# Kernel optimization log

Measured on AMD Instinct MI355X. Metric: run time of the kernel, lower is better.

## Reference

```python
import jax, jax.numpy as jnp
import numpy as np

TOP_K = 8
NEG_SLOPE = 0.2  # PyG GATConv default negative_slope


def setup_inputs() -> dict:
    key = jax.random.key(0)
    ks = jax.random.split(key, 8)
    B, C, T, D, H, KD = 16, 64, 128, 256, 8, 32
    s = 1.0 / np.sqrt(D)
    return {
        "x": jax.random.normal(ks[0], (B, C, T, D), jnp.float32),
        "static_adj": jax.random.normal(ks[1], (C, C), jnp.float32),
        "w_q": jax.random.normal(ks[2], (KD, D), jnp.float32) * s,
        "w_k": jax.random.normal(ks[3], (KD, D), jnp.float32) * s,
        "gat_lin": jax.random.normal(ks[4], (H * D, D), jnp.float32) * s,  # shared lin_src/lin_dst
        "att_src": jax.random.normal(ks[5], (H, D), jnp.float32) * s,
        "att_dst": jax.random.normal(ks[6], (H, D), jnp.float32) * s,
        "gat_bias": jnp.zeros((D,), jnp.float32),
    }


def reference(x, static_adj, w_q, w_k, gat_lin, att_src, att_dst, gat_bias):
    B, C, T, D = x.shape
    H = att_src.shape[0]
    kd = w_q.shape[0]

    # ---- dynamic adjacency ----
    h = x.mean(axis=2)                                   # [B,C,D] temporal summary
    q = h @ w_q.T                                        # [B,C,KD]
    k = h @ w_k.T                                        # [B,C,KD]
    sim = jnp.einsum('bik,bjk->bij', q, k) / np.float32(np.sqrt(kd))
    delta_a = jnp.tanh(sim)                              # [B,C,C]
    adaptive = static_adj[None] + delta_a                # [B,C,C]

    # top-k per row -> sparse mask (edge: row i = source, col j = target, per dense_to_sparse)
    _, idx = jax.lax.top_k(jnp.abs(adaptive), TOP_K)     # [B,C,K]
    mask = jnp.any(jax.nn.one_hot(idx, C, dtype=bool), axis=-2)  # [B,C,C]
    mask = mask | jnp.eye(C, dtype=bool)                 # GATConv add_self_loops=True

    # ---- GAT message passing (dense masked attention, graph shared across T) ----
    xt = jnp.swapaxes(x, 1, 2)                           # [B,T,C,D]
    wx = (xt @ gat_lin.T).reshape(B, T, C, H, D)         # [B,T,C,H,F]
    a_s = jnp.einsum('btchf,hf->btch', wx, att_src)      # source term
    a_d = jnp.einsum('btchf,hf->btch', wx, att_dst)      # target term
    # e[b,t,i,j,h]: edge source i -> target j
    e = a_s[:, :, :, None, :] + a_d[:, :, None, :, :]
    e = jax.nn.leaky_relu(e, NEG_SLOPE)
    e = jnp.where(mask[:, None, :, :, None], e, -jnp.inf)
    alpha = jax.nn.softmax(e, axis=2)                    # softmax over incoming sources i per target j
    out = jnp.einsum('btijh,btihf->btjhf', alpha, wx)    # aggregate messages
    out = out.mean(axis=3) + gat_bias                    # concat=False -> mean heads, add bias
    x_updated = jnp.swapaxes(out, 1, 2)                  # [B,C,T,D]
    return x_updated, delta_a
```

## Files before the change

### kernel.cpp

```cpp
#include <hip/hip_runtime.h>

typedef _Float16 h2_t __attribute__((ext_vector_type(2)));
typedef _Float16 h4_t __attribute__((ext_vector_type(4)));
typedef _Float16 h8_t __attribute__((ext_vector_type(8)));
typedef __fp16 fp16x2 __attribute__((ext_vector_type(2)));
typedef float f32x16 __attribute__((ext_vector_type(16)));


__device__ __forceinline__ h2_t pkrtz(float a, float b) {
  union { fp16x2 f; h2_t h; } u;
  u.f = __builtin_amdgcn_cvt_pkrtz(a, b);
  return u.h;
}

__device__ __forceinline__ unsigned pk_u(float a, float b) {
  union { fp16x2 f; unsigned u; } z;
  z.f = __builtin_amdgcn_cvt_pkrtz(a, b);
  return z.u;
}

__device__ __forceinline__ h8_t mk8(unsigned w0, unsigned w1, unsigned w2, unsigned w3) {
  union { unsigned u[4]; h8_t h; } z;
  z.u[0] = w0; z.u[1] = w1; z.u[2] = w2; z.u[3] = w3;
  return z.h;
}

__device__ __forceinline__ float fdot2_(h2_t a, h2_t b, float c) {
#if __has_builtin(__builtin_amdgcn_fdot2)
  return __builtin_amdgcn_fdot2(a, b, c, false);
#else
  return fmaf((float)a[0], (float)b[0], fmaf((float)a[1], (float)b[1], c));
#endif
}

__device__ __forceinline__ h2_t u2h(unsigned u) {
  union { unsigned u; h2_t h; } x; x.u = u; return x.h;
}

__global__ void k_hmean(const float* __restrict__ x, float* __restrict__ h) {
  __shared__ float4 red[256];
  int bc = blockIdx.x;
  int d4 = threadIdx.x & 63;
  int tq = threadIdx.x >> 6;
  const float4* xp = (const float4*)(x + (size_t)bc * 32768) + d4;
  float4 s = {0.f, 0.f, 0.f, 0.f};
  #pragma unroll 8
  for (int t = 0; t < 32; ++t) {
    float4 v = xp[(size_t)(tq * 32 + t) * 64];
    s.x += v.x; s.y += v.y; s.z += v.z; s.w += v.w;
  }
  red[threadIdx.x] = s;
  __syncthreads();
  if (tq == 0) {
    float4 a = red[d4], b = red[64 + d4], c = red[128 + d4], d = red[192 + d4];
    float4 o;
    o.x = (a.x + b.x + c.x + d.x) * (1.f / 128.f);
    o.y = (a.y + b.y + c.y + d.y) * (1.f / 128.f);
    o.z = (a.z + b.z + c.z + d.z) * (1.f / 128.f);
    o.w = (a.w + b.w + c.w + d.w) * (1.f / 128.f);
    ((float4*)(h + bc * 256))[d4] = o;
  }
}

__global__ void k_qk(const float* __restrict__ h, const float* __restrict__ wq,
                     const float* __restrict__ wk, float* __restrict__ q,
                     float* __restrict__ k) {
  int gid = blockIdx.x * 256 + threadIdx.x;
  int isK = gid >> 15;
  int e = gid & 32767;
  int kk = e & 31;
  int bi = e >> 5;
  const float4* h4 = (const float4*)(h + bi * 256);
  const float4* w4 = (const float4*)((isK ? wk : wq) + kk * 256);
  float s = 0.f;
  #pragma unroll 4
  for (int d = 0; d < 64; ++d) {
    float4 a = h4[d], bv = w4[d];
    s = fmaf(a.x, bv.x, s); s = fmaf(a.y, bv.y, s);
    s = fmaf(a.z, bv.z, s); s = fmaf(a.w, bv.w, s);
  }
  (isK ? k : q)[e] = s;
}

__global__ void k_adj(const float* __restrict__ q, const float* __restrict__ k,
                      const float* __restrict__ sadj, float* __restrict__ dout,
                      unsigned long long* __restrict__ cmask) {
  __shared__ float qs[64][33], ks[64][33];
  __shared__ float ad[64][65];
  __shared__ unsigned long long rowm[64];
  int b = blockIdx.x, tid = threadIdx.x;
  for (int r = 0; r < 8; ++r) {
    int idx = r * 256 + tid;
    qs[idx >> 5][idx & 31] = q[b * 2048 + idx];
    ks[idx >> 5][idx & 31] = k[b * 2048 + idx];
  }
  __syncthreads();
  const float rs = 0.17677669529663687f;
  for (int r = 0; r < 16; ++r) {
    int idx = r * 256 + tid;
    int i = idx >> 6, j = idx & 63;
    float s = 0.f;
    #pragma unroll 8
    for (int kk = 0; kk < 32; ++kk) s = fmaf(qs[i][kk], ks[j][kk], s);
    float dv = tanhf(s * rs);
    dout[b * 4096 + idx] = dv;
    ad[i][j] = sadj[idx] + dv;
  }
  __syncthreads();
  if (tid < 64) {
    unsigned long long sel = 0ull;
    for (int p = 0; p < 8; ++p) {
      float best = -1.f; int bj = 0;
      for (int j = 0; j < 64; ++j) {
        if ((sel >> j) & 1ull) continue;
        float v = fabsf(ad[tid][j]);
        if (v > best) { best = v; bj = j; }
      }
      sel |= 1ull << bj;
    }
    rowm[tid] = sel;
  }
  __syncthreads();
  if (tid < 64) {
    unsigned long long cmv = 1ull << tid;
    for (int i = 0; i < 64; ++i) cmv |= ((rowm[i] >> tid) & 1ull) << i;
    cmask[b * 64 + tid] = cmv;
  }
}

__global__ void k_vsd(const float* __restrict__ glin, const float* __restrict__ asrc,
                      const float* __restrict__ adst, _Float16* __restrict__ vsd16) {
  int hh = blockIdx.x, d = threadIdx.x;
  const float* gb = glin + (size_t)hh * 65536;
  float s = 0.f, t = 0.f;
  for (int f = 0; f < 256; ++f) {
    float g = gb[f * 256 + d];
    s = fmaf(asrc[hh * 256 + f], g, s);
    t = fmaf(adst[hh * 256 + f], g, t);
  }
  vsd16[hh * 256 + d] = (_Float16)s;
  vsd16[(8 + hh) * 256 + d] = (_Float16)t;
}

__global__ void k_grearr(const float* __restrict__ g, _Float16* __restrict__ o) {
  int gid = blockIdx.x * 256 + threadIdx.x;
  int lane = gid & 63;
  int fg = (gid >> 6) & 3;
  int FID = gid >> 8;
  int ft = FID & 1, kk = (FID >> 1) & 3, s = FID >> 3;
  int h = s >> 2, dc = s & 3;
  int l5 = lane & 31, hi = lane >> 5;
  int f = fg * 64 + ft * 32 + l5;
  int d0 = dc * 64 + kk * 16 + hi * 8;
  const float* src = g + ((size_t)(h * 256 + f) << 8) + d0;
  float4 a = *(const float4*)src;
  float4 bq = *(const float4*)(src + 4);
  h8_t v;
  v[0] = (_Float16)a.x;  v[1] = (_Float16)a.y;  v[2] = (_Float16)a.z;  v[3] = (_Float16)a.w;
  v[4] = (_Float16)bq.x; v[5] = (_Float16)bq.y; v[6] = (_Float16)bq.z; v[7] = (_Float16)bq.w;
  *(h8_t*)(o + (size_t)gid * 8) = v;
}

__global__ __launch_bounds__(512) void k_main(
    const float* __restrict__ x, const _Float16* __restrict__ vsd16,
    const unsigned long long* __restrict__ cmask,
    const _Float16* __restrict__ g16r, const float* __restrict__ bias,
    float* __restrict__ out)
{
  __shared__ __align__(16) char LDS[69632];
  char* XR  = LDS;
  char* PT  = LDS;
  char* RED = LDS;
  float* ASp = (float*)(LDS + 65536);
  float* ADp = (float*)(LDS + 67584);

  const int tid = threadIdx.x;
  const int lane = tid & 63;
  const int w = __builtin_amdgcn_readfirstlane(tid >> 6);
  const int hi = lane >> 5;
  const int l5 = lane & 31;
  const int l7 = lane & 7;
  const int mg = w & 1;
  const int fg = w >> 1;
  const int bt = blockIdx.x;
  const int b = bt >> 7, t = bt & 127;

  const char* gb0 = (const char*)g16r + fg * 1024 + lane * 16;

  h8_t GA[8], GB[8];
  #pragma unroll
  for (int q = 0; q < 8; ++q) GA[q] = *(const h8_t*)(gb0 + q * 4096);

  #pragma unroll
  for (int r = 0; r < 8; ++r) {
    int i = w * 8 + r;
    const float4 v = *(const float4*)(x + (((size_t)(b * 64 + i) * 128 + t) << 8) + lane * 4);
    h2_t p0 = pkrtz(v.x, v.y);
    h2_t p1 = pkrtz(v.z, v.w);
    h4_t hv; hv[0] = p0[0]; hv[1] = p0[1]; hv[2] = p1[0]; hv[3] = p1[1];
    int db = lane >> 1;
    int off = i * 512 + (((db & 24) | ((db ^ (i & 7)) & 7)) << 4) + ((lane & 1) << 3);
    *(h4_t*)(XR + off) = hv;
  }
  __syncthreads();

  h8_t Af[16];
  {
    int i = mg * 32 + l5;
    #pragma unroll
    for (int k = 0; k < 16; ++k) {
      int db = k * 2 + hi;
      Af[k] = *(const h8_t*)(XR + i * 512 + (((db & 24) | ((db ^ l7) & 7)) << 4));
    }
  }

  {
    float a_s = 0.f, a_d = 0.f;
    const unsigned* vsp = (const unsigned*)vsd16 + w * 128;
    const unsigned* vdp = (const unsigned*)vsd16 + (8 + w) * 128;
    #pragma unroll 4
    for (int db = 0; db < 32; ++db) {
      h8_t xv = *(const h8_t*)(XR + lane * 512 + (((db & 24) | ((db ^ l7) & 7)) << 4));
      #pragma unroll
      for (int c = 0; c < 4; ++c) {
        h2_t x2; x2[0] = xv[c * 2]; x2[1] = xv[c * 2 + 1];
        a_s = fdot2_(x2, u2h(vsp[db * 4 + c]), a_s);
        a_d = fdot2_(x2, u2h(vdp[db * 4 + c]), a_d);
      }
    }
    ASp[w * 64 + lane] = a_s;
    ADp[w * 64 + lane] = a_d;
  }
  __syncthreads();

  {
    const unsigned long long cmj = cmask[b * 64 + lane];
    const float adj = ADp[w * 64 + lane];
    const float* asr = ASp + w * 64;
    float ssum = 0.f;
    #pragma unroll 8
    for (int i = 0; i < 64; ++i) {
      float e = asr[i] + adj;
      e = fmaxf(e, 0.f) + 0.2f * fminf(e, 0.f);
      e = ((cmj >> i) & 1ull) ? e : -1e30f;
      ssum += exp2f(e * 1.44269504f);
    }
    const float rinv = 1.f / ssum;
    #pragma unroll
    for (int c = 0; c < 8; ++c) {
      float vv[8];
      #pragma unroll
      for (int e8 = 0; e8 < 8; ++e8) {
        int i = c * 8 + e8;
        float e = asr[i] + adj;
        e = fmaxf(e, 0.f) + 0.2f * fminf(e, 0.f);
        e = ((cmj >> i) & 1ull) ? e : -1e30f;
        vv[e8] = exp2f(e * 1.44269504f) * rinv;
      }
      *(h8_t*)(PT + w * 8192 + lane * 128 + ((c ^ l7) << 4)) =
          mk8(pk_u(vv[0], vv[1]), pk_u(vv[2], vv[3]),
              pk_u(vv[4], vv[5]), pk_u(vv[6], vv[7]));
    }
  }
  __syncthreads();

  f32x16 acc00 = {}, acc01 = {}, acc10 = {}, acc11 = {};

  #pragma unroll 1
  for (int h = 0; h < 8; ++h) {
    f32x16 d0 = {}, d1 = {};

    #pragma unroll
    for (int dc = 0; dc < 4; ++dc) {
      const int s = h * 4 + dc;
      const int sp = (s < 31) ? s + 1 : 31;
      const char* gpp = gb0 + (size_t)sp * 32768;
      if ((dc & 1) == 0) {
        #pragma unroll
        for (int q = 0; q < 8; ++q) GB[q] = *(const h8_t*)(gpp + q * 4096);
        __builtin_amdgcn_s_setprio(1);
        #pragma unroll
        for (int kk = 0; kk < 4; ++kk) {
          d0 = __builtin_amdgcn_mfma_f32_32x32x16_f16(Af[dc * 4 + kk], GA[kk * 2 + 0], d0, 0, 0, 0);
          d1 = __builtin_amdgcn_mfma_f32_32x32x16_f16(Af[dc * 4 + kk], GA[kk * 2 + 1], d1, 0, 0, 0);
        }
        __builtin_amdgcn_s_setprio(0);
      } else {
        #pragma unroll
        for (int q = 0; q < 8; ++q) GA[q] = *(const h8_t*)(gpp + q * 4096);
        __builtin_amdgcn_s_setprio(1);
        #pragma unroll
        for (int kk = 0; kk < 4; ++kk) {
          d0 = __builtin_amdgcn_mfma_f32_32x32x16_f16(Af[dc * 4 + kk], GB[kk * 2 + 0], d0, 0, 0, 0);
          d1 = __builtin_amdgcn_mfma_f32_32x32x16_f16(Af[dc * 4 + kk], GB[kk * 2 + 1], d1, 0, 0, 0);
        }
        __builtin_amdgcn_s_setprio(0);
      }
    }

    h8_t B2[2][2];
    {
      const bool H = (hi != 0);
      #pragma unroll
      for (int ft = 0; ft < 2; ++ft) {
        const f32x16& dd = ft ? d1 : d0;
        unsigned P0 = pk_u(dd[0], dd[1]),  P1 = pk_u(dd[2], dd[3]);
        unsigned P2 = pk_u(dd[4], dd[5]),  P3 = pk_u(dd[6], dd[7]);
        unsigned P4 = pk_u(dd[8], dd[9]),  P5 = pk_u(dd[10], dd[11]);
        unsigned P6 = pk_u(dd[12], dd[13]), P7 = pk_u(dd[14], dd[15]);
        {
          unsigned Pa = H ? P2 : P0, Pb = H ? P3 : P1;
          unsigned Qa = H ? P0 : P2, Qb = H ? P1 : P3;
          unsigned S0 = (unsigned)__shfl_xor((int)Qa, 32);
          unsigned S1 = (unsigned)__shfl_xor((int)Qb, 32);
          B2[0][ft] = mk8(H ? S0 : Pa, H ? S1 : Pb, H ? Pa : S0, H ? Pb : S1);
        }
        {
          unsigned Pa = H ? P6 : P4, Pb = H ? P7 : P5;
          unsigned Qa = H ? P4 : P6, Qb = H ? P5 : P7;
          unsigned S0 = (unsigned)__shfl_xor((int)Qa, 32);
          unsigned S1 = (unsigned)__shfl_xor((int)Qb, 32);
          B2[1][ft] = mk8(H ? S0 : Pa, H ? S1 : Pb, H ? Pa : S0, H ? Pb : S1);
        }
      }
    }

    h8_t A2[2][2];
    #pragma unroll
    for (int jt = 0; jt < 2; ++jt)
      #pragma unroll
      for (int kbl = 0; kbl < 2; ++kbl) {
        int c = mg * 4 + kbl * 2 + hi;
        A2[jt][kbl] = *(const h8_t*)(PT + h * 8192 + (jt * 32 + l5) * 128 + ((c ^ (l5 & 7)) << 4));
      }

    __builtin_amdgcn_s_setprio(1);
    acc00 = __builtin_amdgcn_mfma_f32_32x32x16_f16(A2[0][0], B2[0][0], acc00, 0, 0, 0);
    acc00 = __builtin_amdgcn_mfma_f32_32x32x16_f16(A2[0][1], B2[1][0], acc00, 0, 0, 0);
    acc01 = __builtin_amdgcn_mfma_f32_32x32x16_f16(A2[0][0], B2[0][1], acc01, 0, 0, 0);
    acc01 = __builtin_amdgcn_mfma_f32_32x32x16_f16(A2[0][1], B2[1][1], acc01, 0, 0, 0);
    acc10 = __builtin_amdgcn_mfma_f32_32x32x16_f16(A2[1][0], B2[0][0], acc10, 0, 0, 0);
    acc10 = __builtin_amdgcn_mfma_f32_32x32x16_f16(A2[1][1], B2[1][0], acc10, 0, 0, 0);
    acc11 = __builtin_amdgcn_mfma_f32_32x32x16_f16(A2[1][0], B2[0][1], acc11, 0, 0, 0);
    acc11 = __builtin_amdgcn_mfma_f32_32x32x16_f16(A2[1][1], B2[1][1], acc11, 0, 0, 0);
    __builtin_amdgcn_s_setprio(0);
  }

  __syncthreads();
  if (mg == 1) {
    #pragma unroll
    for (int jt = 0; jt < 2; ++jt)
      #pragma unroll
      for (int ft = 0; ft < 2; ++ft) {
        const f32x16& a = jt ? (ft ? acc11 : acc10) : (ft ? acc01 : acc00);
        #pragma unroll
        for (int rq = 0; rq < 4; ++rq) {
          float4 v; v.x = a[rq*4+0]; v.y = a[rq*4+1]; v.z = a[rq*4+2]; v.w = a[rq*4+3];
          *(float4*)(RED + (((((fg*2+jt)*2+ft)*4 + rq)*64 + lane) << 4)) = v;
        }
      }
  }
  __syncthreads();
  if (mg == 0) {
    const float bi0 = bias[fg * 64 + l5];
    const float bi1 = bias[fg * 64 + 32 + l5];
    float* ob = out + ((size_t)(b * 64) * 128 + t) * 256;
    #pragma unroll
    for (int jt = 0; jt < 2; ++jt)
      #pragma unroll
      for (int ft = 0; ft < 2; ++ft) {
        const f32x16& a = jt ? (ft ? acc11 : acc10) : (ft ? acc01 : acc00);
        const float bv = ft ? bi1 : bi0;
        const int fcol = fg * 64 + ft * 32 + l5;
        #pragma unroll
        for (int rq = 0; rq < 4; ++rq) {
          float4 p = *(const float4*)(RED + (((((fg*2+jt)*2+ft)*4 + rq)*64 + lane) << 4));
          #pragma unroll
          for (int rr = 0; rr < 4; ++rr) {
            int j = jt * 32 + rr + 8 * rq + 4 * hi;
            float sum = a[rq*4+rr] + ((const float*)&p)[rr];
            ob[(size_t)j * 32768 + fcol] = sum * 0.125f + bv;
          }
        }
      }
  }
}

extern "C" void kernel_launch(void* const* d_in, const int* in_sizes, int n_in,
                              void* d_out, int out_size, void* d_ws, size_t ws_size,
                              hipStream_t stream) {
  const float* x    = (const float*)d_in[0];
  const float* sadj = (const float*)d_in[1];
  const float* wq   = (const float*)d_in[2];
  const float* wk   = (const float*)d_in[3];
  const float* glin = (const float*)d_in[4];
  const float* asrc = (const float*)d_in[5];
  const float* adst = (const float*)d_in[6];
  const float* bias = (const float*)d_in[7];

  float* out = (float*)d_out;
  float* delta_out = out + (size_t)16 * 64 * 128 * 256;

  char* ws = (char*)d_ws;
  float* h   = (float*)(ws + 0);
  float* q   = (float*)(ws + 1048576);
  float* k   = (float*)(ws + 1179648);
  unsigned long long* cm = (unsigned long long*)(ws + 1310720);
  _Float16* vsd16 = (_Float16*)(ws + 1318912);
  _Float16* g16r  = (_Float16*)(ws + 1327104);

  hipLaunchKernelGGL(k_hmean,  dim3(1024), dim3(256), 0, stream, x, h);
  hipLaunchKernelGGL(k_qk,     dim3(256),  dim3(256), 0, stream, h, wq, wk, q, k);
  hipLaunchKernelGGL(k_adj,    dim3(16),   dim3(256), 0, stream, q, k, sadj, delta_out, cm);
  hipLaunchKernelGGL(k_vsd,    dim3(8),    dim3(256), 0, stream, glin, asrc, adst, vsd16);
  hipLaunchKernelGGL(k_grearr, dim3(256),  dim3(256), 0, stream, glin, g16r);
  hipLaunchKernelGGL(k_main,   dim3(2048), dim3(512), 0, stream, x, vsd16, cm, g16r, bias, out);
}
```

Measured before the change: 374.6 us.

## Split work by feature tile per wave to cut registers and drop LDS reduction

Each wave now owns one 32-wide feature tile across all 64 nodes, instead of splitting nodes into two groups that are later summed through LDS. X fragments are read from LDS on demand rather than held in 16 registers, and the double-buffered G prefetch is removed. The softmax tables are built in two rounds of four heads into a separate LDS region, and launch bounds now request 4 waves per SIMD for higher occupancy. The cost is more LDS reads, extra barriers between rounds, and global G loads that are no longer prefetched ahead of the MFMAs.

```diff
diff --git a/kernel.cpp b/kernel.cpp
--- a/kernel.cpp
+++ b/kernel.cpp
@@ -161,7 +161,7 @@
   *(h8_t*)(o + (size_t)gid * 8) = v;
 }
 
-__global__ __launch_bounds__(512) void k_main(
+__global__ __launch_bounds__(512, 4) void k_main(
     const float* __restrict__ x, const _Float16* __restrict__ vsd16,
     const unsigned long long* __restrict__ cmask,
     const _Float16* __restrict__ g16r, const float* __restrict__ bias,
@@ -169,8 +169,7 @@
 {
   __shared__ __align__(16) char LDS[69632];
   char* XR  = LDS;
-  char* PT  = LDS;
-  char* RED = LDS;
+  char* PT  = LDS + 32768;
   float* ASp = (float*)(LDS + 65536);
   float* ADp = (float*)(LDS + 67584);
 
@@ -180,16 +179,14 @@
   const int hi = lane >> 5;
   const int l5 = lane & 31;
   const int l7 = lane & 7;
-  const int mg = w & 1;
   const int fg = w >> 1;
+  const int ft = w & 1;
   const int bt = blockIdx.x;
   const int b = bt >> 7, t = bt & 127;
 
-  const char* gb0 = (const char*)g16r + fg * 1024 + lane * 16;
-
-  h8_t GA[8], GB[8];
-  #pragma unroll
-  for (int q = 0; q < 8; ++q) GA[q] = *(const h8_t*)(gb0 + q * 4096);
+  const char* gb0 = (const char*)g16r + fg * 1024 + ft * 4096 + lane * 16;
+
+  const unsigned long long cmj = cmask[b * 64 + lane];
 
   #pragma unroll
   for (int r = 0; r < 8; ++r) {
@@ -203,16 +200,6 @@
     *(h4_t*)(XR + off) = hv;
   }
   __syncthreads();
-
-  h8_t Af[16];
-  {
-    int i = mg * 32 + l5;
-    #pragma unroll
-    for (int k = 0; k < 16; ++k) {
-      int db = k * 2 + hi;
-      Af[k] = *(const h8_t*)(XR + i * 512 + (((db & 24) | ((db ^ l7) & 7)) << 4));
-    }
-  }
 
   {
     float a_s = 0.f, a_d = 0.f;
@@ -233,155 +220,161 @@
   }
   __syncthreads();
 
-  {
-    const unsigned long long cmj = cmask[b * 64 + lane];
-    const float adj = ADp[w * 64 + lane];
-    const float* asr = ASp + w * 64;
-    float ssum = 0.f;
-    #pragma unroll 8
-    for (int i = 0; i < 64; ++i) {
-      float e = asr[i] + adj;
-      e = fmaxf(e, 0.f) + 0.2f * fminf(e, 0.f);
-      e = ((cmj >> i) & 1ull) ? e : -1e30f;
-      ssum += exp2f(e * 1.44269504f);
-    }
-    const float rinv = 1.f / ssum;
-    #pragma unroll
-    for (int c = 0; c < 8; ++c) {
-      float vv[8];
-      #pragma unroll
-      for (int e8 = 0; e8 < 8; ++e8) {
-        int i = c * 8 + e8;
+  f32x16 acc0 = {}, acc1 = {};
+
+  #pragma unroll 1
+  for (int rnd = 0; rnd < 2; ++rnd) {
+    if (w < 4) {
+      const int h = rnd * 4 + w;
+      const float adj = ADp[h * 64 + lane];
+      const float* asr = ASp + h * 64;
+      float ssum = 0.f;
+      #pragma unroll 8
+      for (int i = 0; i < 64; ++i) {
         float e = asr[i] + adj;
         e = fmaxf(e, 0.f) + 0.2f * fminf(e, 0.f);
         e = ((cmj >> i) & 1ull) ? e : -1e30f;
-        vv[e8] = exp2f(e * 1.44269504f) * rinv;
-      }
-      *(h8_t*)(PT + w * 8192 + lane * 128 + ((c ^ l7) << 4)) =
-          mk8(pk_u(vv[0], vv[1]), pk_u(vv[2], vv[3]),
-              pk_u(vv[4], vv[5]), pk_u(vv[6], vv[7]));
+        ssum += exp2f(e * 1.44269504f);
+      }
+      const float rinv = 1.f / ssum;
+      char* pslot = PT + w * 8192;
+      #pragma unroll
+      for (int c = 0; c < 8; ++c) {
+        float vv[8];
+        #pragma unroll
+        for (int e8 = 0; e8 < 8; ++e8) {
+          int i = c * 8 + e8;
+          float e = asr[i] + adj;
+          e = fmaxf(e, 0.f) + 0.2f * fminf(e, 0.f);
+          e = ((cmj >> i) & 1ull) ? e : -1e30f;
+          vv[e8] = exp2f(e * 1.44269504f) * rinv;
+        }
+        *(h8_t*)(pslot + lane * 128 + ((c ^ l7) << 4)) =
+            mk8(pk_u(vv[0], vv[1]), pk_u(vv[2], vv[3]),
+                pk_u(vv[4], vv[5]), pk_u(vv[6], vv[7]));
+      }
     }
-  }
-  __syncthreads();
-
-  f32x16 acc00 = {}, acc01 = {}, acc10 = {}, acc11 = {};
-
-  #pragma unroll 1
-  for (int h = 0; h < 8; ++h) {
-    f32x16 d0 = {}, d1 = {};
-
-    #pragma unroll
-    for (int dc = 0; dc < 4; ++dc) {
-      const int s = h * 4 + dc;
-      const int sp = (s < 31) ? s + 1 : 31;
-      const char* gpp = gb0 + (size_t)sp * 32768;
-      if ((dc & 1) == 0) {
-        #pragma unroll
-        for (int q = 0; q < 8; ++q) GB[q] = *(const h8_t*)(gpp + q * 4096);
-        __builtin_amdgcn_s_setprio(1);
-        #pragma unroll
-        for (int kk = 0; kk < 4; ++kk) {
-          d0 = __builtin_amdgcn_mfma_f32_32x32x16_f16(Af[dc * 4 + kk], GA[kk * 2 + 0], d0, 0, 0, 0);
-          d1 = __builtin_amdgcn_mfma_f32_32x32x16_f16(Af[dc * 4 + kk], GA[kk * 2 + 1], d1, 0, 0, 0);
-        }
-        __builtin_amdgcn_s_setprio(0);
-      } else {
-        #pragma unroll
-        for (int q = 0; q < 8; ++q) GA[q] = *(const h8_t*)(gpp + q * 4096);
-        __builtin_amdgcn_s_setprio(1);
-        #pragma unroll
-        for (int kk = 0; kk < 4; ++kk) {
-          d0 = __builtin_amdgcn_mfma_f32_32x32x16_f16(Af[dc * 4 + kk], GB[kk * 2 + 0], d0, 0, 0, 0);
-          d1 = __builtin_amdgcn_mfma_f32_32x32x16_f16(Af[dc * 4 + kk], GB[kk * 2 + 1], d1, 0, 0, 0);
-        }
-        __builtin_amdgcn_s_setprio(0);
-      }
-    }
-
-    h8_t B2[2][2];
-    {
-      const bool H = (hi != 0);
+    __syncthreads();
+
+    #pragma unroll 1
+    for (int hh = 0; hh < 4; ++hh) {
+      const int h = rnd * 4 + hh;
+      f32x16 d0 = {}, d1 = {};
+
       #pragma unroll
-      for (int ft = 0; ft < 2; ++ft) {
-        const f32x16& dd = ft ? d1 : d0;
-        unsigned P0 = pk_u(dd[0], dd[1]),  P1 = pk_u(dd[2], dd[3]);
-        unsigned P2 = pk_u(dd[4], dd[5]),  P3 = pk_u(dd[6], dd[7]);
-        unsigned P4 = pk_u(dd[8], dd[9]),  P5 = pk_u(dd[10], dd[11]);
-        unsigned P6 = pk_u(dd[12], dd[13]), P7 = pk_u(dd[14], dd[15]);
+      for (int dc = 0; dc < 4; ++dc) {
+        const int s = h * 4 + dc;
+        const char* gpp = gb0 + (size_t)s * 32768;
+        h8_t G0 = *(const h8_t*)(gpp);
+        h8_t G1 = *(const h8_t*)(gpp + 8192);
+        h8_t G2 = *(const h8_t*)(gpp + 16384);
+        h8_t G3 = *(const h8_t*)(gpp + 24576);
         {
-          unsigned Pa = H ? P2 : P0, Pb = H ? P3 : P1;
-          unsigned Qa = H ? P0 : P2, Qb = H ? P1 : P3;
-          unsigned S0 = (unsigned)__shfl_xor((int)Qa, 32);
-          unsigned S1 = (unsigned)__shfl_xor((int)Qb, 32);
-          B2[0][ft] = mk8(H ? S0 : Pa, H ? S1 : Pb, H ? Pa : S0, H ? Pb : S1);
+          h8_t a0, a1, a2, a3;
+          {
+            int db = dc * 8 + 0 * 2 + hi;
+            a0 = *(const h8_t*)(XR + l5 * 512 + (((db & 24) | ((db ^ l7) & 7)) << 4));
+            db = dc * 8 + 1 * 2 + hi;
+            a1 = *(const h8_t*)(XR + l5 * 512 + (((db & 24) | ((db ^ l7) & 7)) << 4));
+            db = dc * 8 + 2 * 2 + hi;
+            a2 = *(const h8_t*)(XR + l5 * 512 + (((db & 24) | ((db ^ l7) & 7)) << 4));
+            db = dc * 8 + 3 * 2 + hi;
+            a3 = *(const h8_t*)(XR + l5 * 512 + (((db & 24) | ((db ^ l7) & 7)) << 4));
+          }
+          d0 = __builtin_amdgcn_mfma_f32_32x32x16_f16(a0, G0, d0, 0, 0, 0);
+          d0 = __builtin_amdgcn_mfma_f32_32x32x16_f16(a1, G1, d0, 0, 0, 0);
+          d0 = __builtin_amdgcn_mfma_f32_32x32x16_f16(a2, G2, d0, 0, 0, 0);
+          d0 = __builtin_amdgcn_mfma_f32_32x32x16_f16(a3, G3, d0, 0, 0, 0);
         }
         {
-          unsigned Pa = H ? P6 : P4, Pb = H ? P7 : P5;
-          unsigned Qa = H ? P4 : P6, Qb = H ? P5 : P7;
-          unsigned S0 = (unsigned)__shfl_xor((int)Qa, 32);
-          unsigned S1 = (unsigned)__shfl_xor((int)Qb, 32);
-          B2[1][ft] = mk8(H ? S0 : Pa, H ? S1 : Pb, H ? Pa : S0, H ? Pb : S1);
+          h8_t a0, a1, a2, a3;
+          {
+            int db = dc * 8 + 0 * 2 + hi;
+            a0 = *(const h8_t*)(XR + (32 + l5) * 512 + (((db & 24) | ((db ^ l7) & 7)) << 4));
+            db = dc * 8 + 1 * 2 + hi;
+            a1 = *(const h8_t*)(XR + (32 + l5) * 512 + (((db & 24) | ((db ^ l7) & 7)) << 4));
+            db = dc * 8 + 2 * 2 + hi;
+            a2 = *(const h8_t*)(XR + (32 + l5) * 512 + (((db & 24) | ((db ^ l7) & 7)) << 4));
+            db = dc * 8 + 3 * 2 + hi;
+            a3 = *(const h8_t*)(XR + (32 + l5) * 512 + (((db & 24) | ((db ^ l7) & 7)) << 4));
+          }
+          d1 = __builtin_amdgcn_mfma_f32_32x32x16_f16(a0, G0, d1, 0, 0, 0);
+          d1 = __builtin_amdgcn_mfma_f32_32x32x16_f16(a1, G1, d1, 0, 0, 0);
+          d1 = __builtin_amdgcn_mfma_f32_32x32x16_f16(a2, G2, d1, 0, 0, 0);
+          d1 = __builtin_amdgcn_mfma_f32_32x32x16_f16(a3, G3, d1, 0, 0, 0);
         }
       }
+
+      h8_t B20, B21, B22, B23;
+      {
+        const bool H = (hi != 0);
+        {
+          unsigned P0 = pk_u(d0[0], d0[1]),  P1 = pk_u(d0[2], d0[3]);
+          unsigned P2 = pk_u(d0[4], d0[5]),  P3 = pk_u(d0[6], d0[7]);
+          unsigned P4 = pk_u(d0[8], d0[9]),  P5 = pk_u(d0[10], d0[11]);
+          unsigned P6 = pk_u(d0[12], d0[13]), P7 = pk_u(d0[14], d0[15]);
+          {
+            unsigned Pa = H ? P2 : P0, Pb = H ? P3 : P1;
+            unsigned Qa = H ? P0 : P2, Qb = H ? P1 : P3;
+            unsigned S0 = (unsigned)__shfl_xor((int)Qa, 32);
+            unsigned S1 = (unsigned)__shfl_xor((int)Qb, 32);
+            B20 = mk8(H ? S0 : Pa, H ? S1 : Pb, H ? Pa : S0, H ? Pb : S1);
+          }
+          {
+            unsigned Pa = H ? P6 : P4, Pb = H ? P7 : P5;
+            unsigned Qa = H ? P4 : P6, Qb = H ? P5 : P7;
+            unsigned S0 = (unsigned)__shfl_xor((int)Qa, 32);
+            unsigned S1 = (unsigned)__shfl_xor((int)Qb, 32);
+            B21 = mk8(H ? S0 : Pa, H ? S1 : Pb, H ? Pa : S0, H ? Pb : S1);
+          }
+        }
+        {
+          unsigned P0 = pk_u(d1[0], d1[1]),  P1 = pk_u(d1[2], d1[3]);
+          unsigned P2 = pk_u(d1[4], d1[5]),  P3 = pk_u(d1[6], d1[7]);
+          unsigned P4 = pk_u(d1[8], d1[9]),  P5 = pk_u(d1[10], d1[11]);
+          unsigned P6 = pk_u(d1[12], d1[13]), P7 = pk_u(d1[14], d1[15]);
+          {
+            unsigned Pa = H ? P2 : P0, Pb = H ? P3 : P1;
+            unsigned Qa = H ? P0 : P2, Qb = H ? P1 : P3;
+            unsigned S0 = (unsigned)__shfl_xor((int)Qa, 32);
+            unsigned S1 = (unsigned)__shfl_xor((int)Qb, 32);
+            B22 = mk8(H ? S0 : Pa, H ? S1 : Pb, H ? Pa : S0, H ? Pb : S1);
+          }
+          {
+            unsigned Pa = H ? P6 : P4, Pb = H ? P7 : P5;
+            unsigned Qa = H ? P4 : P6, Qb = H ? P5 : P7;
+            unsigned S0 = (unsigned)__shfl_xor((int)Qa, 32);
+            unsigned S1 = (unsigned)__shfl_xor((int)Qb, 32);
+            B23 = mk8(H ? S0 : Pa, H ? S1 : Pb, H ? Pa : S0, H ? Pb : S1);
+          }
+        }
+      }
+
+      const char* pslot = PT + hh * 8192;
+      #pragma unroll
+      for (int kbl = 0; kbl < 4; ++kbl) {
+        const int c = kbl * 2 + hi;
+        h8_t a20 = *(const h8_t*)(pslot + l5 * 128 + ((c ^ (l5 & 7)) << 4));
+        h8_t a21 = *(const h8_t*)(pslot + (32 + l5) * 128 + ((c ^ (l5 & 7)) << 4));
+        const h8_t bb = (kbl == 0) ? B20 : (kbl == 1) ? B21 : (kbl == 2) ? B22 : B23;
+        acc0 = __builtin_amdgcn_mfma_f32_32x32x16_f16(a20, bb, acc0, 0, 0, 0);
+        acc1 = __builtin_amdgcn_mfma_f32_32x32x16_f16(a21, bb, acc1, 0, 0, 0);
+      }
     }
-
-    h8_t A2[2][2];
-    #pragma unroll
-    for (int jt = 0; jt < 2; ++jt)
-      #pragma unroll
-      for (int kbl = 0; kbl < 2; ++kbl) {
-        int c = mg * 4 + kbl * 2 + hi;
-        A2[jt][kbl] = *(const h8_t*)(PT + h * 8192 + (jt * 32 + l5) * 128 + ((c ^ (l5 & 7)) << 4));
-      }
-
-    __builtin_amdgcn_s_setprio(1);
-    acc00 = __builtin_amdgcn_mfma_f32_32x32x16_f16(A2[0][0], B2[0][0], acc00, 0, 0, 0);
-    acc00 = __builtin_amdgcn_mfma_f32_32x32x16_f16(A2[0][1], B2[1][0], acc00, 0, 0, 0);
-    acc01 = __builtin_amdgcn_mfma_f32_32x32x16_f16(A2[0][0], B2[0][1], acc01, 0, 0, 0);
-    acc01 = __builtin_amdgcn_mfma_f32_32x32x16_f16(A2[0][1], B2[1][1], acc01, 0, 0, 0);
-    acc10 = __builtin_amdgcn_mfma_f32_32x32x16_f16(A2[1][0], B2[0][0], acc10, 0, 0, 0);
-    acc10 = __builtin_amdgcn_mfma_f32_32x32x16_f16(A2[1][1], B2[1][0], acc10, 0, 0, 0);
-    acc11 = __builtin_amdgcn_mfma_f32_32x32x16_f16(A2[1][0], B2[0][1], acc11, 0, 0, 0);
-    acc11 = __builtin_amdgcn_mfma_f32_32x32x16_f16(A2[1][1], B2[1][1], acc11, 0, 0, 0);
-    __builtin_amdgcn_s_setprio(0);
-  }
-
-  __syncthreads();
-  if (mg == 1) {
-    #pragma unroll
-    for (int jt = 0; jt < 2; ++jt)
-      #pragma unroll
-      for (int ft = 0; ft < 2; ++ft) {
-        const f32x16& a = jt ? (ft ? acc11 : acc10) : (ft ? acc01 : acc00);
-        #pragma unroll
-        for (int rq = 0; rq < 4; ++rq) {
-          float4 v; v.x = a[rq*4+0]; v.y = a[rq*4+1]; v.z = a[rq*4+2]; v.w = a[rq*4+3];
-          *(float4*)(RED + (((((fg*2+jt)*2+ft)*4 + rq)*64 + lane) << 4)) = v;
-        }
-      }
-  }
-  __syncthreads();
-  if (mg == 0) {
-    const float bi0 = bias[fg * 64 + l5];
-    const float bi1 = bias[fg * 64 + 32 + l5];
+    __syncthreads();
+  }
+
+  {
+    const int fcol = w * 32 + l5;
+    const float bv = bias[fcol];
     float* ob = out + ((size_t)(b * 64) * 128 + t) * 256;
     #pragma unroll
-    for (int jt = 0; jt < 2; ++jt)
+    for (int rq = 0; rq < 4; ++rq)
       #pragma unroll
-      for (int ft = 0; ft < 2; ++ft) {
-        const f32x16& a = jt ? (ft ? acc11 : acc10) : (ft ? acc01 : acc00);
-        const float bv = ft ? bi1 : bi0;
-        const int fcol = fg * 64 + ft * 32 + l5;
-        #pragma unroll
-        for (int rq = 0; rq < 4; ++rq) {
-          float4 p = *(const float4*)(RED + (((((fg*2+jt)*2+ft)*4 + rq)*64 + lane) << 4));
-          #pragma unroll
-          for (int rr = 0; rr < 4; ++rr) {
-            int j = jt * 32 + rr + 8 * rq + 4 * hi;
-            float sum = a[rq*4+rr] + ((const float*)&p)[rr];
-            ob[(size_t)j * 32768 + fcol] = sum * 0.125f + bv;
-          }
-        }
+      for (int rr = 0; rr < 4; ++rr) {
+        int j0 = rq * 8 + hi * 4 + rr;
+        ob[(size_t)j0 * 32768 + fcol]        = acc0[rq * 4 + rr] * 0.125f + bv;
+        ob[(size_t)(32 + j0) * 32768 + fcol] = acc1[rq * 4 + rr] * 0.125f + bv;
       }
   }
 }
```

Result: slower. 737.9 us (+97.0%).

## Fuse q/k projection into adjacency kernel, merge weight prep kernels, drop setprio

Applied to the files above, without the earlier changes.

Folds the q/k projection into the adjacency/top-k kernel, so each of 16 blocks loads its h rows into LDS and computes q and k there instead of in a separate launch. Also merges the weight rearrangement and attention-vector kernels into one launch, and removes the s_setprio hints around the MFMA sequences in the main kernel. The aim is to cut launch overhead and intermediate global traffic. The cost is that the q/k work now runs on only 16 blocks with a large LDS footprint, which can serialize it, and losing the priority hints may change how MFMA work interleaves across waves.

```diff
diff --git a/kernel.cpp b/kernel.cpp
--- a/kernel.cpp
+++ b/kernel.cpp
@@ -62,39 +62,44 @@
   }
 }
 
-__global__ void k_qk(const float* __restrict__ h, const float* __restrict__ wq,
-                     const float* __restrict__ wk, float* __restrict__ q,
-                     float* __restrict__ k) {
-  int gid = blockIdx.x * 256 + threadIdx.x;
-  int isK = gid >> 15;
-  int e = gid & 32767;
-  int kk = e & 31;
-  int bi = e >> 5;
-  const float4* h4 = (const float4*)(h + bi * 256);
-  const float4* w4 = (const float4*)((isK ? wk : wq) + kk * 256);
-  float s = 0.f;
-  #pragma unroll 4
-  for (int d = 0; d < 64; ++d) {
-    float4 a = h4[d], bv = w4[d];
-    s = fmaf(a.x, bv.x, s); s = fmaf(a.y, bv.y, s);
-    s = fmaf(a.z, bv.z, s); s = fmaf(a.w, bv.w, s);
-  }
-  (isK ? k : q)[e] = s;
-}
-
-__global__ void k_adj(const float* __restrict__ q, const float* __restrict__ k,
-                      const float* __restrict__ sadj, float* __restrict__ dout,
-                      unsigned long long* __restrict__ cmask) {
+__global__ void k_adjq(const float* __restrict__ h, const float* __restrict__ wq,
+                       const float* __restrict__ wk, const float* __restrict__ sadj,
+                       float* __restrict__ dout, unsigned long long* __restrict__ cmask) {
+  __shared__ float hs[64][256];
   __shared__ float qs[64][33], ks[64][33];
   __shared__ float ad[64][65];
   __shared__ unsigned long long rowm[64];
   int b = blockIdx.x, tid = threadIdx.x;
-  for (int r = 0; r < 8; ++r) {
-    int idx = r * 256 + tid;
-    qs[idx >> 5][idx & 31] = q[b * 2048 + idx];
-    ks[idx >> 5][idx & 31] = k[b * 2048 + idx];
-  }
-  __syncthreads();
+
+  {
+    const float4* hp = (const float4*)(h + (size_t)b * 16384);
+    #pragma unroll
+    for (int r = 0; r < 16; ++r) {
+      int idx = r * 256 + tid;
+      ((float4*)&hs[idx >> 6][0])[idx & 63] = hp[idx];
+    }
+  }
+  __syncthreads();
+
+  #pragma unroll
+  for (int r = 0; r < 16; ++r) {
+    int e = r * 256 + tid;
+    int isK = e >> 11;
+    int rest = e & 2047;
+    int i = rest >> 5, kk = rest & 31;
+    const float4* hv = (const float4*)&hs[i][0];
+    const float4* wv = (const float4*)((isK ? wk : wq) + kk * 256);
+    float s = 0.f;
+    #pragma unroll 4
+    for (int d = 0; d < 64; ++d) {
+      float4 a = hv[d], bv = wv[d];
+      s = fmaf(a.x, bv.x, s); s = fmaf(a.y, bv.y, s);
+      s = fmaf(a.z, bv.z, s); s = fmaf(a.w, bv.w, s);
+    }
+    (isK ? ks : qs)[i][kk] = s;
+  }
+  __syncthreads();
+
   const float rs = 0.17677669529663687f;
   for (int r = 0; r < 16; ++r) {
     int idx = r * 256 + tid;
@@ -128,37 +133,38 @@
   }
 }
 
-__global__ void k_vsd(const float* __restrict__ glin, const float* __restrict__ asrc,
-                      const float* __restrict__ adst, _Float16* __restrict__ vsd16) {
-  int hh = blockIdx.x, d = threadIdx.x;
-  const float* gb = glin + (size_t)hh * 65536;
-  float s = 0.f, t = 0.f;
-  for (int f = 0; f < 256; ++f) {
-    float g = gb[f * 256 + d];
-    s = fmaf(asrc[hh * 256 + f], g, s);
-    t = fmaf(adst[hh * 256 + f], g, t);
-  }
-  vsd16[hh * 256 + d] = (_Float16)s;
-  vsd16[(8 + hh) * 256 + d] = (_Float16)t;
-}
-
-__global__ void k_grearr(const float* __restrict__ g, _Float16* __restrict__ o) {
-  int gid = blockIdx.x * 256 + threadIdx.x;
-  int lane = gid & 63;
-  int fg = (gid >> 6) & 3;
-  int FID = gid >> 8;
-  int ft = FID & 1, kk = (FID >> 1) & 3, s = FID >> 3;
-  int h = s >> 2, dc = s & 3;
-  int l5 = lane & 31, hi = lane >> 5;
-  int f = fg * 64 + ft * 32 + l5;
-  int d0 = dc * 64 + kk * 16 + hi * 8;
-  const float* src = g + ((size_t)(h * 256 + f) << 8) + d0;
-  float4 a = *(const float4*)src;
-  float4 bq = *(const float4*)(src + 4);
-  h8_t v;
-  v[0] = (_Float16)a.x;  v[1] = (_Float16)a.y;  v[2] = (_Float16)a.z;  v[3] = (_Float16)a.w;
-  v[4] = (_Float16)bq.x; v[5] = (_Float16)bq.y; v[6] = (_Float16)bq.z; v[7] = (_Float16)bq.w;
-  *(h8_t*)(o + (size_t)gid * 8) = v;
+__global__ void k_prep(const float* __restrict__ g, const float* __restrict__ asrc,
+                       const float* __restrict__ adst, _Float16* __restrict__ o,
+                       _Float16* __restrict__ vsd16) {
+  if (blockIdx.x < 256) {
+    int gid = blockIdx.x * 256 + threadIdx.x;
+    int lane = gid & 63;
+    int fg = (gid >> 6) & 3;
+    int FID = gid >> 8;
+    int ft = FID & 1, kk = (FID >> 1) & 3, s = FID >> 3;
+    int h = s >> 2, dc = s & 3;
+    int l5 = lane & 31, hi = lane >> 5;
+    int f = fg * 64 + ft * 32 + l5;
+    int d0 = dc * 64 + kk * 16 + hi * 8;
+    const float* src = g + ((size_t)(h * 256 + f) << 8) + d0;
+    float4 a = *(const float4*)src;
+    float4 bq = *(const float4*)(src + 4);
+    h8_t v;
+    v[0] = (_Float16)a.x;  v[1] = (_Float16)a.y;  v[2] = (_Float16)a.z;  v[3] = (_Float16)a.w;
+    v[4] = (_Float16)bq.x; v[5] = (_Float16)bq.y; v[6] = (_Float16)bq.z; v[7] = (_Float16)bq.w;
+    *(h8_t*)(o + (size_t)gid * 8) = v;
+  } else {
+    int hh = blockIdx.x - 256, d = threadIdx.x;
+    const float* gb = g + (size_t)hh * 65536;
+    float s = 0.f, t = 0.f;
+    for (int f = 0; f < 256; ++f) {
+      float gv = gb[f * 256 + d];
+      s = fmaf(asrc[hh * 256 + f], gv, s);
+      t = fmaf(adst[hh * 256 + f], gv, t);
+    }
+    vsd16[hh * 256 + d] = (_Float16)s;
+    vsd16[(8 + hh) * 256 + d] = (_Float16)t;
+  }
 }
 
 __global__ __launch_bounds__(512) void k_main(
@@ -278,23 +284,19 @@
       if ((dc & 1) == 0) {
         #pragma unroll
         for (int q = 0; q < 8; ++q) GB[q] = *(const h8_t*)(gpp + q * 4096);
-        __builtin_amdgcn_s_setprio(1);
         #pragma unroll
         for (int kk = 0; kk < 4; ++kk) {
           d0 = __builtin_amdgcn_mfma_f32_32x32x16_f16(Af[dc * 4 + kk], GA[kk * 2 + 0], d0, 0, 0, 0);
           d1 = __builtin_amdgcn_mfma_f32_32x32x16_f16(Af[dc * 4 + kk], GA[kk * 2 + 1], d1, 0, 0, 0);
         }
-        __builtin_amdgcn_s_setprio(0);
       } else {
         #pragma unroll
         for (int q = 0; q < 8; ++q) GA[q] = *(const h8_t*)(gpp + q * 4096);
-        __builtin_amdgcn_s_setprio(1);
         #pragma unroll
         for (int kk = 0; kk < 4; ++kk) {
           d0 = __builtin_amdgcn_mfma_f32_32x32x16_f16(Af[dc * 4 + kk], GB[kk * 2 + 0], d0, 0, 0, 0);
           d1 = __builtin_amdgcn_mfma_f32_32x32x16_f16(Af[dc * 4 + kk], GB[kk * 2 + 1], d1, 0, 0, 0);
         }
-        __builtin_amdgcn_s_setprio(0);
       }
     }
 
@@ -334,7 +336,6 @@
         A2[jt][kbl] = *(const h8_t*)(PT + h * 8192 + (jt * 32 + l5) * 128 + ((c ^ (l5 & 7)) << 4));
       }
 
-    __builtin_amdgcn_s_setprio(1);
     acc00 = __builtin_amdgcn_mfma_f32_32x32x16_f16(A2[0][0], B2[0][0], acc00, 0, 0, 0);
     acc00 = __builtin_amdgcn_mfma_f32_32x32x16_f16(A2[0][1], B2[1][0], acc00, 0, 0, 0);
     acc01 = __builtin_amdgcn_mfma_f32_32x32x16_f16(A2[0][0], B2[0][1], acc01, 0, 0, 0);
@@ -343,7 +344,6 @@
     acc10 = __builtin_amdgcn_mfma_f32_32x32x16_f16(A2[1][1], B2[1][0], acc10, 0, 0, 0);
     acc11 = __builtin_amdgcn_mfma_f32_32x32x16_f16(A2[1][0], B2[0][1], acc11, 0, 0, 0);
     acc11 = __builtin_amdgcn_mfma_f32_32x32x16_f16(A2[1][1], B2[1][1], acc11, 0, 0, 0);
-    __builtin_amdgcn_s_setprio(0);
   }
 
   __syncthreads();
@@ -403,16 +403,12 @@
 
   char* ws = (char*)d_ws;
   float* h   = (float*)(ws + 0);
-  float* q   = (float*)(ws + 1048576);
-  float* k   = (float*)(ws + 1179648);
   unsigned long long* cm = (unsigned long long*)(ws + 1310720);
   _Float16* vsd16 = (_Float16*)(ws + 1318912);
   _Float16* g16r  = (_Float16*)(ws + 1327104);
 
-  hipLaunchKernelGGL(k_hmean,  dim3(1024), dim3(256), 0, stream, x, h);
-  hipLaunchKernelGGL(k_qk,     dim3(256),  dim3(256), 0, stream, h, wq, wk, q, k);
-  hipLaunchKernelGGL(k_adj,    dim3(16),   dim3(256), 0, stream, q, k, sadj, delta_out, cm);
-  hipLaunchKernelGGL(k_vsd,    dim3(8),    dim3(256), 0, stream, glin, asrc, adst, vsd16);
-  hipLaunchKernelGGL(k_grearr, dim3(256),  dim3(256), 0, stream, glin, g16r);
-  hipLaunchKernelGGL(k_main,   dim3(2048), dim3(512), 0, stream, x, vsd16, cm, g16r, bias, out);
-}
+  hipLaunchKernelGGL(k_hmean, dim3(1024), dim3(256), 0, stream, x, h);
+  hipLaunchKernelGGL(k_adjq,  dim3(16),   dim3(256), 0, stream, h, wq, wk, sadj, delta_out, cm);
+  hipLaunchKernelGGL(k_prep,  dim3(264),  dim3(256), 0, stream, glin, asrc, adst, g16r, vsd16);
+  hipLaunchKernelGGL(k_main,  dim3(2048), dim3(512), 0, stream, x, vsd16, cm, g16r, bias, out);
+}
```

After: 459.5 us. 22.7% more time.
